# Kernel optimization log

Hardware: AMD Instinct MI355X
Metric: run time of the kernel (lower is better)

## Reference

```python
import jax, jax.numpy as jnp
import numpy as np

N_HARMONIC = 6
CONCAT = (3,)  # cfg.append_distance: concat embedding after this layer index
N_LAYERS = 8


def harmonic_embedding(x):
    # x: [N, 3] -> [N, 6*2*3 + 3] = [N, 39]
    freqs = 2.0 ** jnp.arange(N_HARMONIC, dtype=x.dtype)  # omega0 = 1.0, logspace
    embed = (x[..., None] * freqs).reshape(*x.shape[:-1], -1)  # [N, 18]
    return jnp.concatenate([jnp.sin(embed), jnp.cos(embed), x], axis=-1)


def setup_inputs() -> dict:
    key = jax.random.key(0)
    N, H, E = 262144, 256, 39
    ks = jax.random.split(key, 11)
    inp = {"points": jax.random.normal(ks[0], (N, 3), dtype=jnp.float32)}
    in_dims = [E, H, H, H, E + H, H, H, H]  # skip-concat before layer 4
    for i, d_in in enumerate(in_dims):
        scale = 1.0 / np.sqrt(d_in)
        inp[f"w{i}"] = jax.random.normal(ks[i + 1], (d_in, H), dtype=jnp.float32) * scale
        inp[f"b{i}"] = jnp.zeros((H,), dtype=jnp.float32)
    inp["wsdf"] = jax.random.normal(ks[9], (H, 1), dtype=jnp.float32) * (1.0 / np.sqrt(H))
    inp["bsdf"] = jnp.zeros((1,), dtype=jnp.float32)
    return inp


def reference(points, w0, b0, w1, b1, w2, b2, w3, b3, w4, b4, w5, b5, w6, b6, w7, b7, wsdf, bsdf):
    ws = [w0, w1, w2, w3, w4, w5, w6, w7]
    bs = [b0, b1, b2, b3, b4, b5, b6, b7]
    emb = harmonic_embedding(points.reshape(-1, 3))  # [N, 39]
    x = emb
    for i in range(N_LAYERS):
        x = jax.nn.relu(x @ ws[i] + bs[i])
        if i in CONCAT:
            x = jnp.concatenate([emb, x], axis=-1)  # torch.cat([add, xyz])
    return x @ wsdf + bsdf  # [N, 1] signed distance
```

## Files before the change

kernel.cpp:

```cpp
#include <hip/hip_runtime.h>
#include <hip/hip_fp16.h>

typedef _Float16 f16x8 __attribute__((ext_vector_type(8)));
typedef _Float16 f16x4 __attribute__((ext_vector_type(4)));
typedef _Float16 f16x2 __attribute__((ext_vector_type(2)));
typedef float    f32x16 __attribute__((ext_vector_type(16)));
typedef float    f32x4 __attribute__((ext_vector_type(4)));

#define SH 264
#define SE 56
#define PTS 128

struct LayerPtrs {
  const float* w[8];
  const float* b[8];
};

__global__ void prep_weights(LayerPtrs P, f16x8* __restrict__ wf) {
  int gid = blockIdx.x * 256 + threadIdx.x;
  if (gid >= 60416) return;
  const int OFF[9] = {0,1536,9728,17920,26112,35840,44032,52224,60416};
  int l = 0;
  while (gid >= OFF[l+1]) ++l;
  int f = gid - OFF[l];
  int lane = f & 63;
  int t = f >> 6;
  int mtile = t & 7;
  int kc = t >> 3;
  int col = mtile * 32 + (lane & 31);
  int kb  = (lane >> 5) * 8;
  const float* w = P.w[l];
  f16x8 v;
#pragma unroll
  for (int j = 0; j < 8; ++j) {
    float x = 0.f;
    if (l == 4) {
      if (kc < 3) {
        int k = kc * 16 + kb + j;
        if (k < 39) x = w[k * 256 + col];
      } else {
        int k = (kc - 3) * 16 + kb + j;
        x = w[(39 + k) * 256 + col];
      }
    } else if (l == 0) {
      int k = kc * 16 + kb + j;
      if (k < 39) x = w[k * 256 + col];
    } else {
      int k = kc * 16 + kb + j;
      x = w[k * 256 + col];
    }
    v[j] = (_Float16)x;
  }
  wf[gid] = v;
}

struct WPre  { f16x8 a0, a1; };
struct BTile { f32x16 t[2]; };

__device__ __forceinline__ WPre wpre(const f16x8* __restrict__ wb) {
  WPre p; p.a0 = wb[0]; p.a1 = wb[64]; return p;
}

__device__ __forceinline__ BTile bias_tile(const float* __restrict__ bp, int h) {
  BTile r;
#pragma unroll
  for (int mt = 0; mt < 2; ++mt)
#pragma unroll
    for (int g = 0; g < 4; ++g) {
      f32x4 q = *(const f32x4*)&bp[mt * 32 + 8 * g + 4 * h];
#pragma unroll
      for (int rr = 0; rr < 4; ++rr) r.t[mt][4 * g + rr] = q[rr];
    }
  return r;
}

#define MFMA __builtin_amdgcn_mfma_f32_32x32x16_f16

template<int NKC, bool FIRST, bool PRE, bool PIPE>
__device__ __forceinline__ void mm(const f16x8* __restrict__ wb,
                                   const _Float16* __restrict__ b0,
                                   const _Float16* __restrict__ b1,
                                   const _Float16* __restrict__ b2,
                                   const _Float16* __restrict__ b3,
                                   f32x16 acc[2][4], const BTile& bt, WPre p) {
  if (PIPE) {
    f16x8 a0 = PRE ? p.a0 : wb[0];
    f16x8 a1 = PRE ? p.a1 : wb[64];
    f16x8 v0 = *(const f16x8*)(b0);
    f16x8 v1 = *(const f16x8*)(b1);
    f16x8 v2 = *(const f16x8*)(b2);
    f16x8 v3 = *(const f16x8*)(b3);
#pragma unroll
    for (int kc = 0; kc < NKC; ++kc) {
      f16x8 na0, na1, nv0, nv1, nv2, nv3;
      if (kc + 1 < NKC) {
        na0 = wb[((kc + 1) * 8 + 0) * 64];
        na1 = wb[((kc + 1) * 8 + 1) * 64];
        nv0 = *(const f16x8*)(b0 + (kc + 1) * 16);
        nv1 = *(const f16x8*)(b1 + (kc + 1) * 16);
        nv2 = *(const f16x8*)(b2 + (kc + 1) * 16);
        nv3 = *(const f16x8*)(b3 + (kc + 1) * 16);
      }
      if (FIRST && kc == 0) {
        acc[0][0] = MFMA(a0, v0, bt.t[0], 0, 0, 0);
        acc[0][1] = MFMA(a0, v1, bt.t[0], 0, 0, 0);
        acc[0][2] = MFMA(a0, v2, bt.t[0], 0, 0, 0);
        acc[0][3] = MFMA(a0, v3, bt.t[0], 0, 0, 0);
        acc[1][0] = MFMA(a1, v0, bt.t[1], 0, 0, 0);
        acc[1][1] = MFMA(a1, v1, bt.t[1], 0, 0, 0);
        acc[1][2] = MFMA(a1, v2, bt.t[1], 0, 0, 0);
        acc[1][3] = MFMA(a1, v3, bt.t[1], 0, 0, 0);
      } else {
        acc[0][0] = MFMA(a0, v0, acc[0][0], 0, 0, 0);
        acc[0][1] = MFMA(a0, v1, acc[0][1], 0, 0, 0);
        acc[0][2] = MFMA(a0, v2, acc[0][2], 0, 0, 0);
        acc[0][3] = MFMA(a0, v3, acc[0][3], 0, 0, 0);
        acc[1][0] = MFMA(a1, v0, acc[1][0], 0, 0, 0);
        acc[1][1] = MFMA(a1, v1, acc[1][1], 0, 0, 0);
        acc[1][2] = MFMA(a1, v2, acc[1][2], 0, 0, 0);
        acc[1][3] = MFMA(a1, v3, acc[1][3], 0, 0, 0);
      }
      if (kc + 1 < NKC) {
        a0 = na0; a1 = na1;
        v0 = nv0; v1 = nv1; v2 = nv2; v3 = nv3;
      }
    }
  } else {
#pragma unroll
    for (int kc = 0; kc < NKC; ++kc) {
      f16x8 a0 = (PRE && kc == 0) ? p.a0 : wb[(kc * 8 + 0) * 64];
      f16x8 a1 = (PRE && kc == 0) ? p.a1 : wb[(kc * 8 + 1) * 64];
      f16x8 v0 = *(const f16x8*)(b0 + kc * 16);
      f16x8 v1 = *(const f16x8*)(b1 + kc * 16);
      f16x8 v2 = *(const f16x8*)(b2 + kc * 16);
      f16x8 v3 = *(const f16x8*)(b3 + kc * 16);
      if (FIRST && kc == 0) {
        acc[0][0] = MFMA(a0, v0, bt.t[0], 0, 0, 0);
        acc[0][1] = MFMA(a0, v1, bt.t[0], 0, 0, 0);
        acc[0][2] = MFMA(a0, v2, bt.t[0], 0, 0, 0);
        acc[0][3] = MFMA(a0, v3, bt.t[0], 0, 0, 0);
        acc[1][0] = MFMA(a1, v0, bt.t[1], 0, 0, 0);
        acc[1][1] = MFMA(a1, v1, bt.t[1], 0, 0, 0);
        acc[1][2] = MFMA(a1, v2, bt.t[1], 0, 0, 0);
        acc[1][3] = MFMA(a1, v3, bt.t[1], 0, 0, 0);
      } else {
        acc[0][0] = MFMA(a0, v0, acc[0][0], 0, 0, 0);
        acc[0][1] = MFMA(a0, v1, acc[0][1], 0, 0, 0);
        acc[0][2] = MFMA(a0, v2, acc[0][2], 0, 0, 0);
        acc[0][3] = MFMA(a0, v3, acc[0][3], 0, 0, 0);
        acc[1][0] = MFMA(a1, v0, acc[1][0], 0, 0, 0);
        acc[1][1] = MFMA(a1, v1, acc[1][1], 0, 0, 0);
        acc[1][2] = MFMA(a1, v2, acc[1][2], 0, 0, 0);
        acc[1][3] = MFMA(a1, v3, acc[1][3], 0, 0, 0);
      }
    }
  }
}

__device__ __forceinline__ f16x4 relu_cvt4(float a0, float a1, float a2, float a3) {
  f16x2 lo = __builtin_bit_cast(f16x2, __builtin_amdgcn_cvt_pkrtz(a0, a1));
  f16x2 hi = __builtin_bit_cast(f16x2, __builtin_amdgcn_cvt_pkrtz(a2, a3));
  union { f16x4 v; f16x2 h[2]; } u;
  u.h[0] = lo; u.h[1] = hi;
  f16x4 z = {};
  return __builtin_elementwise_max(u.v, z);
}

__device__ __forceinline__ void store_act(f32x16 acc[2][4], int wg,
                                          int lane, _Float16* __restrict__ H) {
  int p0 = lane & 31, h = lane >> 5;
#pragma unroll
  for (int mt = 0; mt < 2; ++mt) {
    int hb = wg * 64 + mt * 32 + 4 * h;
#pragma unroll
    for (int g = 0; g < 4; ++g) {
#pragma unroll
      for (int nt = 0; nt < 4; ++nt) {
        f16x4 o = relu_cvt4(acc[mt][nt][4 * g + 0], acc[mt][nt][4 * g + 1],
                            acc[mt][nt][4 * g + 2], acc[mt][nt][4 * g + 3]);
        *(f16x4*)&H[(nt * 32 + p0) * SH + hb + 8 * g] = o;
      }
    }
  }
}

__global__ __launch_bounds__(256, 2)
void mlp_fused(const float* __restrict__ points,
               LayerPtrs P,
               const f16x8* __restrict__ wf,
               const float* __restrict__ wsdf,
               const float* __restrict__ bsdf,
               float* __restrict__ out) {
  __shared__ __align__(16) _Float16 H[PTS * SH];
  __shared__ __align__(16) _Float16 E[PTS * SE];
  const int tid = threadIdx.x;
  const int blk = blockIdx.x;

  const int lane = tid & 63;
  const int wg   = tid >> 6;
  const int p0   = lane & 31;
  const int h    = lane >> 5;

  const f16x8* wb = wf + (wg * 2) * 64 + lane;
  const int WOFF[8] = {0,1536,9728,17920,26112,35840,44032,52224};

  WPre  wp = wpre(wb + WOFF[0]);
  BTile bt = bias_tile(P.b[0] + wg * 64, h);

  if (tid < PTS) {
    int p = blk * PTS + tid;
    float xyz[3] = {points[p * 3 + 0], points[p * 3 + 1], points[p * 3 + 2]};
    _Float16* row = &E[tid * SE];
#pragma unroll
    for (int c = 0; c < 3; ++c) {
      float fr = 1.f;
#pragma unroll
      for (int k = 0; k < 6; ++k) {
        float e = xyz[c] * fr;
        row[c * 6 + k]      = (_Float16)sinf(e);
        row[18 + c * 6 + k] = (_Float16)cosf(e);
        fr *= 2.f;
      }
      row[36 + c] = (_Float16)xyz[c];
    }
#pragma unroll
    for (int c = 39; c < SE; ++c) row[c] = (_Float16)0.f;
  }
  __syncthreads();

  const _Float16* e0 = &E[p0 * SE + h * 8];
  const _Float16* e1 = &E[(32 + p0) * SE + h * 8];
  const _Float16* e2 = &E[(64 + p0) * SE + h * 8];
  const _Float16* e3 = &E[(96 + p0) * SE + h * 8];
  const _Float16* h0 = &H[p0 * SH + h * 8];
  const _Float16* h1 = &H[(32 + p0) * SH + h * 8];
  const _Float16* h2 = &H[(64 + p0) * SH + h * 8];
  const _Float16* h3 = &H[(96 + p0) * SH + h * 8];

  f32x16 acc[2][4];

  mm<3, true, true, true>(wb + WOFF[0], e0, e1, e2, e3, acc, bt, wp);
  bt = bias_tile(P.b[1] + wg * 64, h);
  wp = wpre(wb + WOFF[1]);
  store_act(acc, wg, lane, H);
  __syncthreads();

#pragma unroll
  for (int l = 1; l < 4; ++l) {
    mm<16, true, true, true>(wb + WOFF[l], h0, h1, h2, h3, acc, bt, wp);
    bt = bias_tile(P.b[l + 1] + wg * 64, h);
    wp = wpre(wb + WOFF[l + 1]);
    __syncthreads();
    store_act(acc, wg, lane, H);
    __syncthreads();
  }

  mm<3, true, true, true>(wb + WOFF[4], e0, e1, e2, e3, acc, bt, wp);
  mm<16, false, false, true>(wb + WOFF[4] + 3 * 512, h0, h1, h2, h3, acc, bt, wp);
  bt = bias_tile(P.b[5] + wg * 64, h);
  wp = wpre(wb + WOFF[5]);
  __syncthreads();
  store_act(acc, wg, lane, H);
  __syncthreads();

#pragma unroll
  for (int l = 5; l < 7; ++l) {
    mm<16, true, true, true>(wb + WOFF[l], h0, h1, h2, h3, acc, bt, wp);
    bt = bias_tile(P.b[l + 1] + wg * 64, h);
    wp = wpre(wb + WOFF[l + 1]);
    __syncthreads();
    store_act(acc, wg, lane, H);
    __syncthreads();
  }

  mm<16, true, true, false>(wb + WOFF[7], h0, h1, h2, h3, acc, bt, wp);
  {
    float part[4] = {0.f, 0.f, 0.f, 0.f};
#pragma unroll
    for (int mt = 0; mt < 2; ++mt)
#pragma unroll
      for (int g = 0; g < 4; ++g) {
        f32x4 q = *(const f32x4*)&wsdf[wg * 64 + mt * 32 + 8 * g + 4 * h];
#pragma unroll
        for (int nt = 0; nt < 4; ++nt)
#pragma unroll
          for (int r = 0; r < 4; ++r)
            part[nt] += fmaxf(acc[mt][nt][4 * g + r], 0.f) * q[r];
      }
    float* PB = (float*)E;
    __syncthreads();
#pragma unroll
    for (int nt = 0; nt < 4; ++nt)
      PB[(wg * 2 + h) * 128 + nt * 32 + p0] = part[nt];
    __syncthreads();
    if (tid < PTS) {
      float s = bsdf[0];
#pragma unroll
      for (int j = 0; j < 8; ++j) s += PB[j * 128 + tid];
      out[blk * PTS + tid] = s;
    }
  }
}

extern "C" void kernel_launch(void* const* d_in, const int* in_sizes, int n_in,
                              void* d_out, int out_size, void* d_ws, size_t ws_size,
                              hipStream_t stream) {
  const float* points = (const float*)d_in[0];
  LayerPtrs P;
  for (int i = 0; i < 8; ++i) {
    P.w[i] = (const float*)d_in[1 + 2 * i];
    P.b[i] = (const float*)d_in[2 + 2 * i];
  }
  const float* wsdf = (const float*)d_in[17];
  const float* bsdf = (const float*)d_in[18];
  f16x8* wf = (f16x8*)d_ws;

  int N = in_sizes[0] / 3;
  prep_weights<<<236, 256, 0, stream>>>(P, wf);
  mlp_fused<<<N / PTS, 256, 0, stream>>>(points, P, wf, wsdf, bsdf, (float*)d_out);
}
```

Measured before the change: 307.4 us.

## Split work across 8 waves with XOR-swizzled LDS and epilogue bias

Doubles the block to 512 threads, with each wave covering 64 hidden units by 64 points instead of 64 by 128. This halves the accumulator registers per wave so more waves can be resident. LDS padding is replaced by an XOR swizzle on row offsets to avoid bank conflicts. The bias add moves from the MFMA accumulator init into the store epilogue, and weight prefetch goes two k-steps ahead. The embedding is computed across more threads using fast __sinf/__cosf, which lowers precision for large arguments.

```diff
diff --git a/kernel.cpp b/kernel.cpp
--- a/kernel.cpp
+++ b/kernel.cpp
@@ -6,10 +6,6 @@
 typedef _Float16 f16x2 __attribute__((ext_vector_type(2)));
 typedef float    f32x16 __attribute__((ext_vector_type(16)));
 typedef float    f32x4 __attribute__((ext_vector_type(4)));
-
-#define SH 264
-#define SE 56
-#define PTS 128
 
 struct LayerPtrs {
   const float* w[8];
@@ -54,106 +50,54 @@
   wf[gid] = v;
 }
 
-struct WPre  { f16x8 a0, a1; };
-struct BTile { f32x16 t[2]; };
-
-__device__ __forceinline__ WPre wpre(const f16x8* __restrict__ wb) {
-  WPre p; p.a0 = wb[0]; p.a1 = wb[64]; return p;
-}
-
-__device__ __forceinline__ BTile bias_tile(const float* __restrict__ bp, int h) {
-  BTile r;
-#pragma unroll
-  for (int mt = 0; mt < 2; ++mt)
-#pragma unroll
-    for (int g = 0; g < 4; ++g) {
-      f32x4 q = *(const f32x4*)&bp[mt * 32 + 8 * g + 4 * h];
-#pragma unroll
-      for (int rr = 0; rr < 4; ++rr) r.t[mt][4 * g + rr] = q[rr];
-    }
-  return r;
-}
-
 #define MFMA __builtin_amdgcn_mfma_f32_32x32x16_f16
 
-template<int NKC, bool FIRST, bool PRE, bool PIPE>
+struct WPre2 { f16x8 a00, a01, a10, a11; };
+
+__device__ __forceinline__ WPre2 wpre2(const f16x8* __restrict__ wb) {
+  WPre2 p;
+  p.a00 = wb[0];   p.a01 = wb[64];
+  p.a10 = wb[512]; p.a11 = wb[576];
+  return p;
+}
+
+template<int NKC, bool FIRST, int RSTRIDE, bool PRE>
 __device__ __forceinline__ void mm(const f16x8* __restrict__ wb,
-                                   const _Float16* __restrict__ b0,
-                                   const _Float16* __restrict__ b1,
-                                   const _Float16* __restrict__ b2,
-                                   const _Float16* __restrict__ b3,
-                                   f32x16 acc[2][4], const BTile& bt, WPre p) {
-  if (PIPE) {
-    f16x8 a0 = PRE ? p.a0 : wb[0];
-    f16x8 a1 = PRE ? p.a1 : wb[64];
-    f16x8 v0 = *(const f16x8*)(b0);
-    f16x8 v1 = *(const f16x8*)(b1);
-    f16x8 v2 = *(const f16x8*)(b2);
-    f16x8 v3 = *(const f16x8*)(b3);
-#pragma unroll
-    for (int kc = 0; kc < NKC; ++kc) {
-      f16x8 na0, na1, nv0, nv1, nv2, nv3;
-      if (kc + 1 < NKC) {
-        na0 = wb[((kc + 1) * 8 + 0) * 64];
-        na1 = wb[((kc + 1) * 8 + 1) * 64];
-        nv0 = *(const f16x8*)(b0 + (kc + 1) * 16);
-        nv1 = *(const f16x8*)(b1 + (kc + 1) * 16);
-        nv2 = *(const f16x8*)(b2 + (kc + 1) * 16);
-        nv3 = *(const f16x8*)(b3 + (kc + 1) * 16);
-      }
-      if (FIRST && kc == 0) {
-        acc[0][0] = MFMA(a0, v0, bt.t[0], 0, 0, 0);
-        acc[0][1] = MFMA(a0, v1, bt.t[0], 0, 0, 0);
-        acc[0][2] = MFMA(a0, v2, bt.t[0], 0, 0, 0);
-        acc[0][3] = MFMA(a0, v3, bt.t[0], 0, 0, 0);
-        acc[1][0] = MFMA(a1, v0, bt.t[1], 0, 0, 0);
-        acc[1][1] = MFMA(a1, v1, bt.t[1], 0, 0, 0);
-        acc[1][2] = MFMA(a1, v2, bt.t[1], 0, 0, 0);
-        acc[1][3] = MFMA(a1, v3, bt.t[1], 0, 0, 0);
-      } else {
-        acc[0][0] = MFMA(a0, v0, acc[0][0], 0, 0, 0);
-        acc[0][1] = MFMA(a0, v1, acc[0][1], 0, 0, 0);
-        acc[0][2] = MFMA(a0, v2, acc[0][2], 0, 0, 0);
-        acc[0][3] = MFMA(a0, v3, acc[0][3], 0, 0, 0);
-        acc[1][0] = MFMA(a1, v0, acc[1][0], 0, 0, 0);
-        acc[1][1] = MFMA(a1, v1, acc[1][1], 0, 0, 0);
-        acc[1][2] = MFMA(a1, v2, acc[1][2], 0, 0, 0);
-        acc[1][3] = MFMA(a1, v3, acc[1][3], 0, 0, 0);
-      }
-      if (kc + 1 < NKC) {
-        a0 = na0; a1 = na1;
-        v0 = nv0; v1 = nv1; v2 = nv2; v3 = nv3;
-      }
-    }
-  } else {
-#pragma unroll
-    for (int kc = 0; kc < NKC; ++kc) {
-      f16x8 a0 = (PRE && kc == 0) ? p.a0 : wb[(kc * 8 + 0) * 64];
-      f16x8 a1 = (PRE && kc == 0) ? p.a1 : wb[(kc * 8 + 1) * 64];
-      f16x8 v0 = *(const f16x8*)(b0 + kc * 16);
-      f16x8 v1 = *(const f16x8*)(b1 + kc * 16);
-      f16x8 v2 = *(const f16x8*)(b2 + kc * 16);
-      f16x8 v3 = *(const f16x8*)(b3 + kc * 16);
-      if (FIRST && kc == 0) {
-        acc[0][0] = MFMA(a0, v0, bt.t[0], 0, 0, 0);
-        acc[0][1] = MFMA(a0, v1, bt.t[0], 0, 0, 0);
-        acc[0][2] = MFMA(a0, v2, bt.t[0], 0, 0, 0);
-        acc[0][3] = MFMA(a0, v3, bt.t[0], 0, 0, 0);
-        acc[1][0] = MFMA(a1, v0, bt.t[1], 0, 0, 0);
-        acc[1][1] = MFMA(a1, v1, bt.t[1], 0, 0, 0);
-        acc[1][2] = MFMA(a1, v2, bt.t[1], 0, 0, 0);
-        acc[1][3] = MFMA(a1, v3, bt.t[1], 0, 0, 0);
-      } else {
-        acc[0][0] = MFMA(a0, v0, acc[0][0], 0, 0, 0);
-        acc[0][1] = MFMA(a0, v1, acc[0][1], 0, 0, 0);
-        acc[0][2] = MFMA(a0, v2, acc[0][2], 0, 0, 0);
-        acc[0][3] = MFMA(a0, v3, acc[0][3], 0, 0, 0);
-        acc[1][0] = MFMA(a1, v0, acc[1][0], 0, 0, 0);
-        acc[1][1] = MFMA(a1, v1, acc[1][1], 0, 0, 0);
-        acc[1][2] = MFMA(a1, v2, acc[1][2], 0, 0, 0);
-        acc[1][3] = MFMA(a1, v3, acc[1][3], 0, 0, 0);
-      }
-    }
+                                   const char* __restrict__ r0,
+                                   int col0, int xr,
+                                   f32x16 acc[2][2], WPre2 wp) {
+  f16x8 a00, a01, a10, a11;
+  if (PRE) { a00 = wp.a00; a01 = wp.a01; a10 = wp.a10; a11 = wp.a11; }
+  else     { a00 = wb[0];  a01 = wb[64]; a10 = wb[512]; a11 = wb[576]; }
+  int off0 = col0 ^ xr;
+  f16x8 v0 = *(const f16x8*)(r0 + off0);
+  f16x8 v1 = *(const f16x8*)(r0 + RSTRIDE + off0);
+#pragma unroll
+  for (int kc = 0; kc < NKC; ++kc) {
+    f16x8 n0, n1, nv0, nv1;
+    if (kc + 2 < NKC) {
+      n0 = wb[(kc + 2) * 512];
+      n1 = wb[(kc + 2) * 512 + 64];
+    }
+    if (kc + 1 < NKC) {
+      int off = (col0 + 32 * (kc + 1)) ^ xr;
+      nv0 = *(const f16x8*)(r0 + off);
+      nv1 = *(const f16x8*)(r0 + RSTRIDE + off);
+    }
+    if (FIRST && kc == 0) {
+      const f32x16 z = {};
+      acc[0][0] = MFMA(a00, v0, z, 0, 0, 0);
+      acc[0][1] = MFMA(a00, v1, z, 0, 0, 0);
+      acc[1][0] = MFMA(a01, v0, z, 0, 0, 0);
+      acc[1][1] = MFMA(a01, v1, z, 0, 0, 0);
+    } else {
+      acc[0][0] = MFMA(a00, v0, acc[0][0], 0, 0, 0);
+      acc[0][1] = MFMA(a00, v1, acc[0][1], 0, 0, 0);
+      acc[1][0] = MFMA(a01, v0, acc[1][0], 0, 0, 0);
+      acc[1][1] = MFMA(a01, v1, acc[1][1], 0, 0, 0);
+    }
+    a00 = a10; a01 = a11; a10 = n0; a11 = n1;
+    v0 = nv0; v1 = nv1;
   }
 }
 
@@ -166,138 +110,152 @@
   return __builtin_elementwise_max(u.v, z);
 }
 
-__device__ __forceinline__ void store_act(f32x16 acc[2][4], int wg,
-                                          int lane, _Float16* __restrict__ H) {
-  int p0 = lane & 31, h = lane >> 5;
+__device__ __forceinline__ void store_epi(f32x16 acc[2][2],
+                                          const float* __restrict__ bias,
+                                          int wg_h, int wg_p, int p0, int h,
+                                          int xr, _Float16* __restrict__ Hs) {
+  char* base = (char*)Hs + (wg_p * 64 + p0) * 512;
 #pragma unroll
   for (int mt = 0; mt < 2; ++mt) {
-    int hb = wg * 64 + mt * 32 + 4 * h;
 #pragma unroll
     for (int g = 0; g < 4; ++g) {
-#pragma unroll
-      for (int nt = 0; nt < 4; ++nt) {
-        f16x4 o = relu_cvt4(acc[mt][nt][4 * g + 0], acc[mt][nt][4 * g + 1],
-                            acc[mt][nt][4 * g + 2], acc[mt][nt][4 * g + 3]);
-        *(f16x4*)&H[(nt * 32 + p0) * SH + hb + 8 * g] = o;
-      }
-    }
-  }
-}
-
-__global__ __launch_bounds__(256, 2)
+      f32x4 q = *(const f32x4*)&bias[wg_h * 64 + mt * 32 + 8 * g + 4 * h];
+      int bc = (128 * wg_h + 64 * mt + 8 * h + 16 * g) ^ xr;
+#pragma unroll
+      for (int nt = 0; nt < 2; ++nt) {
+        f16x4 o = relu_cvt4(acc[mt][nt][4 * g + 0] + q[0],
+                            acc[mt][nt][4 * g + 1] + q[1],
+                            acc[mt][nt][4 * g + 2] + q[2],
+                            acc[mt][nt][4 * g + 3] + q[3]);
+        *(f16x4*)(base + nt * 32 * 512 + bc) = o;
+      }
+    }
+  }
+}
+
+__global__ __launch_bounds__(512, 4)
 void mlp_fused(const float* __restrict__ points,
                LayerPtrs P,
                const f16x8* __restrict__ wf,
                const float* __restrict__ wsdf,
                const float* __restrict__ bsdf,
                float* __restrict__ out) {
-  __shared__ __align__(16) _Float16 H[PTS * SH];
-  __shared__ __align__(16) _Float16 E[PTS * SE];
+  __shared__ __align__(16) _Float16 Hs[128 * 256];
+  __shared__ __align__(16) _Float16 Es[128 * 64];
   const int tid = threadIdx.x;
   const int blk = blockIdx.x;
 
   const int lane = tid & 63;
-  const int wg   = tid >> 6;
+  const int w    = tid >> 6;
+  const int wg_h = w & 3;
+  const int wg_p = w >> 2;
   const int p0   = lane & 31;
   const int h    = lane >> 5;
-
-  const f16x8* wb = wf + (wg * 2) * 64 + lane;
-  const int WOFF[8] = {0,1536,9728,17920,26112,35840,44032,52224};
-
-  WPre  wp = wpre(wb + WOFF[0]);
-  BTile bt = bias_tile(P.b[0] + wg * 64, h);
-
-  if (tid < PTS) {
-    int p = blk * PTS + tid;
-    float xyz[3] = {points[p * 3 + 0], points[p * 3 + 1], points[p * 3 + 2]};
-    _Float16* row = &E[tid * SE];
-#pragma unroll
-    for (int c = 0; c < 3; ++c) {
+  const int xr   = (p0 & 7) << 4;
+  const int col0 = 16 * h;
+
+  const f16x8* wb = wf + wg_h * 128 + lane;
+
+  WPre2 wp = wpre2(wb);
+
+  {
+    int p = tid & 127, part = tid >> 7;
+    char* Erow = (char*)Es + p * 128;
+    int xp = (p & 7) << 4;
+    if (part < 3) {
+      float x = points[(blk * 128 + p) * 3 + part];
+      _Float16 sv[6], cv[6];
       float fr = 1.f;
 #pragma unroll
       for (int k = 0; k < 6; ++k) {
-        float e = xyz[c] * fr;
-        row[c * 6 + k]      = (_Float16)sinf(e);
-        row[18 + c * 6 + k] = (_Float16)cosf(e);
+        float e = x * fr;
+        sv[k] = (_Float16)__sinf(e);
+        cv[k] = (_Float16)__cosf(e);
         fr *= 2.f;
       }
-      row[36 + c] = (_Float16)xyz[c];
-    }
-#pragma unroll
-    for (int c = 39; c < SE; ++c) row[c] = (_Float16)0.f;
+#pragma unroll
+      for (int k = 0; k < 6; k += 2) {
+        f16x2 s2 = {sv[k], sv[k + 1]};
+        f16x2 c2 = {cv[k], cv[k + 1]};
+        *(f16x2*)(Erow + ((2 * (6 * part + k)) ^ xp)) = s2;
+        *(f16x2*)(Erow + ((2 * (18 + 6 * part + k)) ^ xp)) = c2;
+      }
+      *(_Float16*)(Erow + ((2 * (36 + part)) ^ xp)) = (_Float16)x;
+    } else {
+      f16x4 z4 = {};
+      *(_Float16*)(Erow + (78 ^ xp)) = (_Float16)0.f;
+      *(f16x4*)(Erow + (80 ^ xp)) = z4;
+      *(f16x4*)(Erow + (88 ^ xp)) = z4;
+    }
   }
   __syncthreads();
 
-  const _Float16* e0 = &E[p0 * SE + h * 8];
-  const _Float16* e1 = &E[(32 + p0) * SE + h * 8];
-  const _Float16* e2 = &E[(64 + p0) * SE + h * 8];
-  const _Float16* e3 = &E[(96 + p0) * SE + h * 8];
-  const _Float16* h0 = &H[p0 * SH + h * 8];
-  const _Float16* h1 = &H[(32 + p0) * SH + h * 8];
-  const _Float16* h2 = &H[(64 + p0) * SH + h * 8];
-  const _Float16* h3 = &H[(96 + p0) * SH + h * 8];
-
-  f32x16 acc[2][4];
-
-  mm<3, true, true, true>(wb + WOFF[0], e0, e1, e2, e3, acc, bt, wp);
-  bt = bias_tile(P.b[1] + wg * 64, h);
-  wp = wpre(wb + WOFF[1]);
-  store_act(acc, wg, lane, H);
+  const char* hR = (const char*)Hs + (wg_p * 64 + p0) * 512;
+  const char* eR = (const char*)Es + (wg_p * 64 + p0) * 128;
+
+  f32x16 acc[2][2];
+
+  mm<3, true, 4096, true>(wb, eR, col0, xr, acc, wp);
+  wp = wpre2(wb + 1536);
+  store_epi(acc, P.b[0], wg_h, wg_p, p0, h, xr, Hs);
   __syncthreads();
 
+  const int WOFF[8] = {0, 1536, 9728, 17920, 26112, 35840, 44032, 52224};
+
 #pragma unroll
   for (int l = 1; l < 4; ++l) {
-    mm<16, true, true, true>(wb + WOFF[l], h0, h1, h2, h3, acc, bt, wp);
-    bt = bias_tile(P.b[l + 1] + wg * 64, h);
-    wp = wpre(wb + WOFF[l + 1]);
-    __syncthreads();
-    store_act(acc, wg, lane, H);
-    __syncthreads();
-  }
-
-  mm<3, true, true, true>(wb + WOFF[4], e0, e1, e2, e3, acc, bt, wp);
-  mm<16, false, false, true>(wb + WOFF[4] + 3 * 512, h0, h1, h2, h3, acc, bt, wp);
-  bt = bias_tile(P.b[5] + wg * 64, h);
-  wp = wpre(wb + WOFF[5]);
-  __syncthreads();
-  store_act(acc, wg, lane, H);
-  __syncthreads();
+    mm<16, true, 16384, true>(wb + WOFF[l], hR, col0, xr, acc, wp);
+    wp = wpre2(wb + WOFF[l + 1]);
+    __syncthreads();
+    store_epi(acc, P.b[l], wg_h, wg_p, p0, h, xr, Hs);
+    __syncthreads();
+  }
+
+  {
+    mm<3, true, 4096, true>(wb + 26112, eR, col0, xr, acc, wp);
+    mm<16, false, 16384, false>(wb + 27648, hR, col0, xr, acc, wp);
+    wp = wpre2(wb + 35840);
+    __syncthreads();
+    store_epi(acc, P.b[4], wg_h, wg_p, p0, h, xr, Hs);
+    __syncthreads();
+  }
 
 #pragma unroll
   for (int l = 5; l < 7; ++l) {
-    mm<16, true, true, true>(wb + WOFF[l], h0, h1, h2, h3, acc, bt, wp);
-    bt = bias_tile(P.b[l + 1] + wg * 64, h);
-    wp = wpre(wb + WOFF[l + 1]);
-    __syncthreads();
-    store_act(acc, wg, lane, H);
-    __syncthreads();
-  }
-
-  mm<16, true, true, false>(wb + WOFF[7], h0, h1, h2, h3, acc, bt, wp);
+    mm<16, true, 16384, true>(wb + WOFF[l], hR, col0, xr, acc, wp);
+    wp = wpre2(wb + WOFF[l + 1]);
+    __syncthreads();
+    store_epi(acc, P.b[l], wg_h, wg_p, p0, h, xr, Hs);
+    __syncthreads();
+  }
+
+  mm<16, true, 16384, true>(wb + 52224, hR, col0, xr, acc, wp);
   {
-    float part[4] = {0.f, 0.f, 0.f, 0.f};
-#pragma unroll
-    for (int mt = 0; mt < 2; ++mt)
+    float part0 = 0.f, part1 = 0.f;
+    const float* b7 = P.b[7];
+#pragma unroll
+    for (int mt = 0; mt < 2; ++mt) {
 #pragma unroll
       for (int g = 0; g < 4; ++g) {
-        f32x4 q = *(const f32x4*)&wsdf[wg * 64 + mt * 32 + 8 * g + 4 * h];
-#pragma unroll
-        for (int nt = 0; nt < 4; ++nt)
-#pragma unroll
-          for (int r = 0; r < 4; ++r)
-            part[nt] += fmaxf(acc[mt][nt][4 * g + r], 0.f) * q[r];
-      }
-    float* PB = (float*)E;
-    __syncthreads();
-#pragma unroll
-    for (int nt = 0; nt < 4; ++nt)
-      PB[(wg * 2 + h) * 128 + nt * 32 + p0] = part[nt];
-    __syncthreads();
-    if (tid < PTS) {
+        int idx = wg_h * 64 + mt * 32 + 8 * g + 4 * h;
+        f32x4 qb = *(const f32x4*)&b7[idx];
+        f32x4 qw = *(const f32x4*)&wsdf[idx];
+#pragma unroll
+        for (int r = 0; r < 4; ++r) {
+          part0 += fmaxf(acc[mt][0][4 * g + r] + qb[r], 0.f) * qw[r];
+          part1 += fmaxf(acc[mt][1][4 * g + r] + qb[r], 0.f) * qw[r];
+        }
+      }
+    }
+    float* PB = (float*)Es;
+    PB[(wg_h * 2 + h) * 128 + wg_p * 64 + p0]      = part0;
+    PB[(wg_h * 2 + h) * 128 + wg_p * 64 + 32 + p0] = part1;
+    __syncthreads();
+    if (tid < 128) {
       float s = bsdf[0];
 #pragma unroll
       for (int j = 0; j < 8; ++j) s += PB[j * 128 + tid];
-      out[blk * PTS + tid] = s;
+      out[blk * 128 + tid] = s;
     }
   }
 }
@@ -317,5 +275,5 @@
 
   int N = in_sizes[0] / 3;
   prep_weights<<<236, 256, 0, stream>>>(P, wf);
-  mlp_fused<<<N / PTS, 256, 0, stream>>>(points, P, wf, wsdf, bsdf, (float*)d_out);
-}
+  mlp_fused<<<N / 128, 512, 0, stream>>>(points, P, wf, wsdf, bsdf, (float*)d_out);
+}
```

After: 351.0 us. 1.14x slower.
